# Optimization experiments

Measured on AMD Instinct MI355X. Metric: run time of the kernel, lower is better.

The kernel has to match this reference:

```python
import jax, jax.numpy as jnp
import numpy as np

N, E, D = 100000, 1280000, 64


def setup_inputs() -> dict:
    key = jax.random.key(0)
    ks = jax.random.split(key, 9)
    x = jax.random.normal(ks[0], (N, D), jnp.float32)
    edge_index = jax.random.randint(ks[1], (2, E), 0, N, dtype=jnp.int64)
    edge_weight = jax.random.uniform(ks[2], (E,), jnp.float32)
    s = 1.0 / np.sqrt(D)
    W0 = jax.random.normal(ks[3], (D, D), jnp.float32) * s
    b0 = jnp.zeros((D,), jnp.float32)
    W1 = jax.random.normal(ks[4], (D, D), jnp.float32) * s
    b1 = jnp.zeros((D,), jnp.float32)
    W2 = jax.random.normal(ks[5], (D, D), jnp.float32) * s
    b2 = jnp.zeros((D,), jnp.float32)
    return {"x": x, "edge_index": edge_index, "edge_weight": edge_weight,
            "W0": W0, "b0": b0, "W1": W1, "b1": b1, "W2": W2, "b2": b2}


def reference(x, edge_index, edge_weight, W0, b0, W1, b1, W2, b2):
    n = x.shape[0]
    row, col = edge_index[0], edge_index[1]
    # GCN normalization with self-loops (PyG gcn_norm, fill_value=1)
    loop = jnp.arange(n)
    row_f = jnp.concatenate([row, loop])
    col_f = jnp.concatenate([col, loop])
    w_f = jnp.concatenate([edge_weight, jnp.ones((n,), x.dtype)])
    deg = jax.ops.segment_sum(w_f, col_f, num_segments=n)
    dinv = jnp.where(deg > 0, jax.lax.rsqrt(deg), 0.0).astype(x.dtype)
    norm = dinv[row_f] * w_f * dinv[col_f]  # [E+N]

    def conv(h, W, b):
        h = h @ W                                  # [N, D_out]
        msg = h[row_f] * norm[:, None]             # gather + scale
        return jax.ops.segment_sum(msg, col_f, num_segments=n) + b

    results = [x]
    h = jax.nn.relu(conv(x, W0, b0))   # dropout p=0 / eval -> identity
    results.append(h)
    h = jax.nn.relu(conv(h, W1, b1))
    results.append(h)
    h = conv(h, W2, b2)                # last layer: no activation
    results.append(h)
    return tuple(results)
```

## Files before the change

### kernel.cpp

```cpp
#include <hip/hip_runtime.h>


#define TPB 256
#define P1_CHUNK 8192
#define DSH 7
#define DNB 128
#define STAGE_CAP 4096

__global__ __launch_bounds__(TPB) void k_p0(const int* __restrict__ col,
                                            int* __restrict__ chist, int E, int nbk) {
    __shared__ int h[1024];
    int tid = threadIdx.x;
    for (int i = tid; i < nbk; i += TPB) h[i] = 0;
    __syncthreads();
    int s0 = blockIdx.x * P1_CHUNK;
    int s1 = min(s0 + P1_CHUNK, E);
    for (int i = s0 + tid; i < s1; i += TPB) atomicAdd(&h[col[i] >> DSH], 1);
    __syncthreads();
    for (int i = tid; i < nbk; i += TPB)
        if (h[i]) atomicAdd(&chist[i], h[i]);
}

__global__ __launch_bounds__(1024) void k_scanb(const int* __restrict__ chist,
                                                int* __restrict__ cbase,
                                                int* __restrict__ ccur, int nbk, int E) {
    __shared__ int s[1024];
    int tid = threadIdx.x;
    int v = (tid < nbk) ? chist[tid] : 0;
    s[tid] = v;
    __syncthreads();
    for (int off = 1; off < 1024; off <<= 1) {
        int t = (tid >= off) ? s[tid - off] : 0;
        __syncthreads();
        s[tid] += t;
        __syncthreads();
    }
    if (tid < nbk) { int ex = s[tid] - v; cbase[tid] = ex; ccur[tid] = ex; }
    if (tid == 0) cbase[nbk] = E;
}

__global__ __launch_bounds__(TPB) void k_p1(const int* __restrict__ row,
                                            const int* __restrict__ col,
                                            const float* __restrict__ w,
                                            int* __restrict__ ccur,
                                            int2* __restrict__ bkt, int E, int nbk) {
    __shared__ int h[1024];
    __shared__ int base[1024];
    int tid = threadIdx.x;
    for (int i = tid; i < nbk; i += TPB) h[i] = 0;
    __syncthreads();
    int s0 = blockIdx.x * P1_CHUNK;
    int s1 = min(s0 + P1_CHUNK, E);
    for (int i = s0 + tid; i < s1; i += TPB) atomicAdd(&h[col[i] >> DSH], 1);
    __syncthreads();
    for (int i = tid; i < nbk; i += TPB) {
        int c = h[i];
        base[i] = c ? atomicAdd(&ccur[i], c) : 0;
        h[i] = 0;
    }
    __syncthreads();
    for (int i = s0 + tid; i < s1; i += TPB) {
        int c = col[i];
        int b = c >> DSH;
        int r = atomicAdd(&h[b], 1);
        bkt[base[b] + r] = make_int2(row[i] | ((c & (DNB - 1)) << 20), __float_as_int(w[i]));
    }
}

__global__ __launch_bounds__(TPB) void k_p2(const int2* __restrict__ bkt,
                                            const int* __restrict__ cbase,
                                            int* __restrict__ starts,
                                            int2* __restrict__ edges,
                                            float* __restrict__ dinv, int n, int E) {
    __shared__ int hist[DNB];
    __shared__ int curs[DNB];
    __shared__ int sc[DNB];
    __shared__ int2 stage[STAGE_CAP];
    int tid = threadIdx.x;
    int b = blockIdx.x;
    int s0 = cbase[b], s1 = cbase[b + 1];
    int cnt = s1 - s0;
    int nodeBase = b << DSH;
    if (tid < DNB) hist[tid] = 0;
    __syncthreads();
    for (int i = s0 + tid; i < s1; i += TPB)
        atomicAdd(&hist[(unsigned)bkt[i].x >> 20], 1);
    __syncthreads();
    int v = 0;
    if (tid < DNB) { v = hist[tid]; sc[tid] = v; }
    __syncthreads();
    for (int off = 1; off < DNB; off <<= 1) {
        int t = 0;
        if (tid < DNB && tid >= off) t = sc[tid - off];
        __syncthreads();
        if (tid < DNB) sc[tid] += t;
        __syncthreads();
    }
    if (tid < DNB) {
        int ex = sc[tid] - v;
        curs[tid] = ex;
        int node = nodeBase + tid;
        if (node < n) starts[node] = s0 + ex;
    }
    if (b == 0 && tid == 0) starts[n] = E;
    __syncthreads();
    if (cnt <= STAGE_CAP) {
        for (int i = s0 + tid; i < s1; i += TPB) {
            int2 ed = bkt[i];
            int d = (unsigned)ed.x >> 20;
            int r = atomicAdd(&curs[d], 1);
            stage[r] = make_int2(ed.x & 0xFFFFF, ed.y);
        }
        __syncthreads();
        for (int i = tid; i < cnt; i += TPB) edges[s0 + i] = stage[i];
        if (tid < DNB) {
            int node = nodeBase + tid;
            if (node < n) {
                float d = 1.0f;
                for (int j = sc[tid] - v; j < sc[tid]; ++j)
                    d += __int_as_float(stage[j].y);
                dinv[node] = rsqrtf(d);
            }
        }
    } else {
        for (int i = s0 + tid; i < s1; i += TPB) {
            int2 ed = bkt[i];
            int d = (unsigned)ed.x >> 20;
            int r = atomicAdd(&curs[d], 1);
            edges[s0 + r] = make_int2(ed.x & 0xFFFFF, ed.y);
        }
        __syncthreads();
        if (tid < DNB) {
            int node = nodeBase + tid;
            if (node < n) {
                float d = 1.0f;
                for (int j = sc[tid] - v; j < sc[tid]; ++j)
                    d += __int_as_float(edges[s0 + j].y);
                dinv[node] = rsqrtf(d);
            }
        }
    }
}

__global__ __launch_bounds__(TPB) void k_normcsr(const int* __restrict__ starts,
                                                 const float* __restrict__ dinv,
                                                 int2* __restrict__ edges, int n) {
    int i = blockIdx.x * TPB + threadIdx.x;
    if (i >= n) return;
    int s0 = starts[i], s1 = starts[i + 1];
    float dn = dinv[i];
    for (int s = s0; s < s1; ++s) {
        int2 ed = edges[s];
        edges[s].y = __float_as_int(dinv[ed.x] * __int_as_float(ed.y) * dn);
    }
}

__global__ __launch_bounds__(TPB, 3) void k_gemm64(const float* __restrict__ in,
                                                   const float* __restrict__ Wg,
                                                   float* __restrict__ out, int n) {
    __shared__ float4 Ws[1024];
    __shared__ float4 As[2048];
    int tid = threadIdx.x;
    const float4* Wf4 = (const float4*)Wg;
    #pragma unroll
    for (int i = 0; i < 4; ++i) Ws[i * 256 + tid] = Wf4[i * 256 + tid];
    int rowbase = blockIdx.x * 128;
    const float4* Af4 = (const float4*)in;
    #pragma unroll
    for (int i = 0; i < 8; ++i) {
        int f4 = i * 256 + tid;
        int r = f4 >> 4, c4 = f4 & 15;
        float4 v = make_float4(0.f, 0.f, 0.f, 0.f);
        if (rowbase + r < n) v = Af4[(size_t)(rowbase + r) * 16 + c4];
        As[r * 16 + (c4 ^ ((r >> 3) & 3))] = v;
    }
    __syncthreads();
    int jg = tid & 15;
    int rg = tid >> 4;
    int r0 = rg * 8;
    int sw = rg & 3;
    float4 acc[8];
    #pragma unroll
    for (int rr = 0; rr < 8; ++rr) acc[rr] = make_float4(0.f, 0.f, 0.f, 0.f);
    #pragma unroll 2
    for (int kt = 0; kt < 16; ++kt) {
        float4 w0 = Ws[(kt * 4 + 0) * 16 + jg];
        float4 w1 = Ws[(kt * 4 + 1) * 16 + jg];
        float4 w2 = Ws[(kt * 4 + 2) * 16 + jg];
        float4 w3 = Ws[(kt * 4 + 3) * 16 + jg];
        int ac = kt ^ sw;
        #pragma unroll
        for (int rr = 0; rr < 8; ++rr) {
            float4 a = As[(r0 + rr) * 16 + ac];
            acc[rr].x = fmaf(a.x, w0.x, acc[rr].x);
            acc[rr].y = fmaf(a.x, w0.y, acc[rr].y);
            acc[rr].z = fmaf(a.x, w0.z, acc[rr].z);
            acc[rr].w = fmaf(a.x, w0.w, acc[rr].w);
            acc[rr].x = fmaf(a.y, w1.x, acc[rr].x);
            acc[rr].y = fmaf(a.y, w1.y, acc[rr].y);
            acc[rr].z = fmaf(a.y, w1.z, acc[rr].z);
            acc[rr].w = fmaf(a.y, w1.w, acc[rr].w);
            acc[rr].x = fmaf(a.z, w2.x, acc[rr].x);
            acc[rr].y = fmaf(a.z, w2.y, acc[rr].y);
            acc[rr].z = fmaf(a.z, w2.z, acc[rr].z);
            acc[rr].w = fmaf(a.z, w2.w, acc[rr].w);
            acc[rr].x = fmaf(a.w, w3.x, acc[rr].x);
            acc[rr].y = fmaf(a.w, w3.y, acc[rr].y);
            acc[rr].z = fmaf(a.w, w3.z, acc[rr].z);
            acc[rr].w = fmaf(a.w, w3.w, acc[rr].w);
        }
    }
    #pragma unroll
    for (int rr = 0; rr < 8; ++rr) {
        int r = rowbase + r0 + rr;
        if (r < n) *(float4*)&out[(size_t)r * 64 + jg * 4] = acc[rr];
    }
}

__global__ __launch_bounds__(TPB) void k_gather(const int* __restrict__ starts,
                                                const int2* __restrict__ edges,
                                                const float* __restrict__ hw,
                                                const float* __restrict__ dinv,
                                                const float* __restrict__ b,
                                                float* __restrict__ out,
                                                int n, int relu) {
    int idx = blockIdx.x * TPB + threadIdx.x;
    int node = idx >> 4;
    if (node >= n) return;
    int f = (idx & 15) << 2;
    int s0 = starts[node], s1 = starts[node + 1];
    float di = dinv[node];
    float sc = di * di;
    float4 hself = *(const float4*)&hw[(size_t)node * 64 + f];
    float4 bb = *(const float4*)&b[f];
    float4 acc;
    acc.x = fmaf(hself.x, sc, bb.x);
    acc.y = fmaf(hself.y, sc, bb.y);
    acc.z = fmaf(hself.z, sc, bb.z);
    acc.w = fmaf(hself.w, sc, bb.w);
    int e = s0;
    for (; e + 4 <= s1; e += 4) {
        int2 e0 = edges[e + 0];
        int2 e1 = edges[e + 1];
        int2 e2 = edges[e + 2];
        int2 e3 = edges[e + 3];
        float4 h0 = *(const float4*)&hw[(size_t)e0.x * 64 + f];
        float4 h1 = *(const float4*)&hw[(size_t)e1.x * 64 + f];
        float4 h2 = *(const float4*)&hw[(size_t)e2.x * 64 + f];
        float4 h3 = *(const float4*)&hw[(size_t)e3.x * 64 + f];
        float n0 = __int_as_float(e0.y), n1 = __int_as_float(e1.y);
        float n2 = __int_as_float(e2.y), n3 = __int_as_float(e3.y);
        acc.x = fmaf(h0.x, n0, acc.x); acc.y = fmaf(h0.y, n0, acc.y);
        acc.z = fmaf(h0.z, n0, acc.z); acc.w = fmaf(h0.w, n0, acc.w);
        acc.x = fmaf(h1.x, n1, acc.x); acc.y = fmaf(h1.y, n1, acc.y);
        acc.z = fmaf(h1.z, n1, acc.z); acc.w = fmaf(h1.w, n1, acc.w);
        acc.x = fmaf(h2.x, n2, acc.x); acc.y = fmaf(h2.y, n2, acc.y);
        acc.z = fmaf(h2.z, n2, acc.z); acc.w = fmaf(h2.w, n2, acc.w);
        acc.x = fmaf(h3.x, n3, acc.x); acc.y = fmaf(h3.y, n3, acc.y);
        acc.z = fmaf(h3.z, n3, acc.z); acc.w = fmaf(h3.w, n3, acc.w);
    }
    for (; e < s1; ++e) {
        int2 ed = edges[e];
        float nm = __int_as_float(ed.y);
        float4 h = *(const float4*)&hw[(size_t)ed.x * 64 + f];
        acc.x = fmaf(h.x, nm, acc.x);
        acc.y = fmaf(h.y, nm, acc.y);
        acc.z = fmaf(h.z, nm, acc.z);
        acc.w = fmaf(h.w, nm, acc.w);
    }
    if (relu) {
        acc.x = acc.x > 0.f ? acc.x : 0.f;
        acc.y = acc.y > 0.f ? acc.y : 0.f;
        acc.z = acc.z > 0.f ? acc.z : 0.f;
        acc.w = acc.w > 0.f ? acc.w : 0.f;
    }
    *(float4*)&out[(size_t)node * 64 + f] = acc;
}

extern "C" void kernel_launch(void* const* d_in, const int* in_sizes, int n_in,
                              void* d_out, int out_size, void* d_ws, size_t ws_size,
                              hipStream_t stream) {
    const float* x = (const float*)d_in[0];
    const int* ei = (const int*)d_in[1];
    const float* ew = (const float*)d_in[2];
    const float* Wl[3] = {(const float*)d_in[3], (const float*)d_in[5], (const float*)d_in[7]};
    const float* Bl[3] = {(const float*)d_in[4], (const float*)d_in[6], (const float*)d_in[8]};

    const int n = in_sizes[0] / 64;
    const int E = in_sizes[2];
    const int* row = ei;
    const int* col = ei + E;
    float* out = (float*)d_out;

    const int nbk = (n + DNB - 1) >> DSH;
    const int p1b = (E + P1_CHUNK - 1) / P1_CHUNK;

    char* ws = (char*)d_ws;
    size_t o = 0;
    float* dinv  = (float*)(ws + o);  o = (o + (size_t)n * 4 + 255) & ~(size_t)255;
    float* hw    = (float*)(ws + o);
    int2*  bkt   = (int2*)(ws + o);   o = (o + (size_t)n * 256 + 255) & ~(size_t)255;
    int* starts  = (int*)(ws + o);    o = (o + (size_t)(n + 1) * 4 + 255) & ~(size_t)255;
    int* chist   = (int*)(ws + o);    o = (o + 1024 * 4 + 255) & ~(size_t)255;
    int* cbase   = (int*)(ws + o);    o = (o + 1025 * 4 + 255) & ~(size_t)255;
    int* ccur    = (int*)(ws + o);    o = (o + 1024 * 4 + 255) & ~(size_t)255;
    int2* edges  = (int2*)(ws + o);

    hipMemcpyAsync(out, x, (size_t)n * 64 * sizeof(float), hipMemcpyDeviceToDevice, stream);

    hipMemsetAsync(chist, 0, (size_t)nbk * 4, stream);
    k_p0<<<p1b, TPB, 0, stream>>>(col, chist, E, nbk);
    k_scanb<<<1, 1024, 0, stream>>>(chist, cbase, ccur, nbk, E);
    k_p1<<<p1b, TPB, 0, stream>>>(row, col, ew, ccur, bkt, E, nbk);
    k_p2<<<nbk, TPB, 0, stream>>>(bkt, cbase, starts, edges, dinv, n, E);
    k_normcsr<<<(n + TPB - 1) / TPB, TPB, 0, stream>>>(starts, dinv, edges, n);

    const float* hin = x;
    for (int L = 0; L < 3; ++L) {
        float* oseg = out + (size_t)(L + 1) * n * 64;
        k_gemm64<<<(n + 127) / 128, TPB, 0, stream>>>(hin, Wl[L], hw, n);
        k_gather<<<(n * 16 + TPB - 1) / TPB, TPB, 0, stream>>>(starts, edges, hw, dinv, Bl[L], oseg, n, L < 2 ? 1 : 0);
        hin = oseg;
    }
}
```

Measured before the change: 438.7 us.

## Split gather edges across 4 slots per node, drop normcsr pass and x copy

The gather kernel now gives each node a full 64-lane wavefront, with 4 edge slots of 16 lanes each. The partial sums are combined with cross-lane shuffles. The per-edge normalisation kernel is removed: the source dinv is applied inside the gather and the destination dinv is applied once per node after the reduction, which adds an extra dinv gather per edge. The device-to-device copy of x into the output is folded into the first GEMM's load phase, so the separate memcpy launch and the extra pass over memory go away.

Result: no change. 434.0 us (-1.1%).

```diff
diff --git a/kernel.cpp b/kernel.cpp
--- a/kernel.cpp
+++ b/kernel.cpp
@@ -142,22 +142,10 @@
     }
 }
 
-__global__ __launch_bounds__(TPB) void k_normcsr(const int* __restrict__ starts,
-                                                 const float* __restrict__ dinv,
-                                                 int2* __restrict__ edges, int n) {
-    int i = blockIdx.x * TPB + threadIdx.x;
-    if (i >= n) return;
-    int s0 = starts[i], s1 = starts[i + 1];
-    float dn = dinv[i];
-    for (int s = s0; s < s1; ++s) {
-        int2 ed = edges[s];
-        edges[s].y = __float_as_int(dinv[ed.x] * __int_as_float(ed.y) * dn);
-    }
-}
-
 __global__ __launch_bounds__(TPB, 3) void k_gemm64(const float* __restrict__ in,
                                                    const float* __restrict__ Wg,
-                                                   float* __restrict__ out, int n) {
+                                                   float* __restrict__ out,
+                                                   float* __restrict__ cp, int n) {
     __shared__ float4 Ws[1024];
     __shared__ float4 As[2048];
     int tid = threadIdx.x;
@@ -171,7 +159,10 @@
         int f4 = i * 256 + tid;
         int r = f4 >> 4, c4 = f4 & 15;
         float4 v = make_float4(0.f, 0.f, 0.f, 0.f);
-        if (rowbase + r < n) v = Af4[(size_t)(rowbase + r) * 16 + c4];
+        if (rowbase + r < n) {
+            v = Af4[(size_t)(rowbase + r) * 16 + c4];
+            if (cp) *(float4*)&cp[((size_t)(rowbase + r) * 16 + c4) * 4] = v;
+        }
         As[r * 16 + (c4 ^ ((r >> 3) & 3))] = v;
     }
     __syncthreads();
@@ -224,57 +215,68 @@
                                                 const float* __restrict__ b,
                                                 float* __restrict__ out,
                                                 int n, int relu) {
-    int idx = blockIdx.x * TPB + threadIdx.x;
-    int node = idx >> 4;
+    int node = blockIdx.x * 4 + (threadIdx.x >> 6);
     if (node >= n) return;
-    int f = (idx & 15) << 2;
+    int lane = threadIdx.x & 63;
+    int eslot = lane >> 4;
+    int f = (lane & 15) << 2;
     int s0 = starts[node], s1 = starts[node + 1];
-    float di = dinv[node];
-    float sc = di * di;
-    float4 hself = *(const float4*)&hw[(size_t)node * 64 + f];
-    float4 bb = *(const float4*)&b[f];
-    float4 acc;
-    acc.x = fmaf(hself.x, sc, bb.x);
-    acc.y = fmaf(hself.y, sc, bb.y);
-    acc.z = fmaf(hself.z, sc, bb.z);
-    acc.w = fmaf(hself.w, sc, bb.w);
-    int e = s0;
-    for (; e + 4 <= s1; e += 4) {
-        int2 e0 = edges[e + 0];
-        int2 e1 = edges[e + 1];
-        int2 e2 = edges[e + 2];
-        int2 e3 = edges[e + 3];
-        float4 h0 = *(const float4*)&hw[(size_t)e0.x * 64 + f];
-        float4 h1 = *(const float4*)&hw[(size_t)e1.x * 64 + f];
-        float4 h2 = *(const float4*)&hw[(size_t)e2.x * 64 + f];
-        float4 h3 = *(const float4*)&hw[(size_t)e3.x * 64 + f];
-        float n0 = __int_as_float(e0.y), n1 = __int_as_float(e1.y);
-        float n2 = __int_as_float(e2.y), n3 = __int_as_float(e3.y);
-        acc.x = fmaf(h0.x, n0, acc.x); acc.y = fmaf(h0.y, n0, acc.y);
-        acc.z = fmaf(h0.z, n0, acc.z); acc.w = fmaf(h0.w, n0, acc.w);
-        acc.x = fmaf(h1.x, n1, acc.x); acc.y = fmaf(h1.y, n1, acc.y);
-        acc.z = fmaf(h1.z, n1, acc.z); acc.w = fmaf(h1.w, n1, acc.w);
-        acc.x = fmaf(h2.x, n2, acc.x); acc.y = fmaf(h2.y, n2, acc.y);
-        acc.z = fmaf(h2.z, n2, acc.z); acc.w = fmaf(h2.w, n2, acc.w);
-        acc.x = fmaf(h3.x, n3, acc.x); acc.y = fmaf(h3.y, n3, acc.y);
-        acc.z = fmaf(h3.z, n3, acc.z); acc.w = fmaf(h3.w, n3, acc.w);
-    }
-    for (; e < s1; ++e) {
+    float4 acc = make_float4(0.f, 0.f, 0.f, 0.f);
+    int e = s0 + eslot;
+    for (; e + 4 < s1; e += 8) {
+        int2 ed0 = edges[e];
+        int2 ed1 = edges[e + 4];
+        float nm0 = dinv[ed0.x] * __int_as_float(ed0.y);
+        float nm1 = dinv[ed1.x] * __int_as_float(ed1.y);
+        float4 h0 = *(const float4*)&hw[(size_t)ed0.x * 64 + f];
+        float4 h1 = *(const float4*)&hw[(size_t)ed1.x * 64 + f];
+        acc.x = fmaf(h0.x, nm0, acc.x);
+        acc.y = fmaf(h0.y, nm0, acc.y);
+        acc.z = fmaf(h0.z, nm0, acc.z);
+        acc.w = fmaf(h0.w, nm0, acc.w);
+        acc.x = fmaf(h1.x, nm1, acc.x);
+        acc.y = fmaf(h1.y, nm1, acc.y);
+        acc.z = fmaf(h1.z, nm1, acc.z);
+        acc.w = fmaf(h1.w, nm1, acc.w);
+    }
+    if (e < s1) {
         int2 ed = edges[e];
-        float nm = __int_as_float(ed.y);
+        float nm = dinv[ed.x] * __int_as_float(ed.y);
         float4 h = *(const float4*)&hw[(size_t)ed.x * 64 + f];
         acc.x = fmaf(h.x, nm, acc.x);
         acc.y = fmaf(h.y, nm, acc.y);
         acc.z = fmaf(h.z, nm, acc.z);
         acc.w = fmaf(h.w, nm, acc.w);
     }
-    if (relu) {
-        acc.x = acc.x > 0.f ? acc.x : 0.f;
-        acc.y = acc.y > 0.f ? acc.y : 0.f;
-        acc.z = acc.z > 0.f ? acc.z : 0.f;
-        acc.w = acc.w > 0.f ? acc.w : 0.f;
-    }
-    *(float4*)&out[(size_t)node * 64 + f] = acc;
+    acc.x += __shfl_xor(acc.x, 16);
+    acc.y += __shfl_xor(acc.y, 16);
+    acc.z += __shfl_xor(acc.z, 16);
+    acc.w += __shfl_xor(acc.w, 16);
+    acc.x += __shfl_xor(acc.x, 32);
+    acc.y += __shfl_xor(acc.y, 32);
+    acc.z += __shfl_xor(acc.z, 32);
+    acc.w += __shfl_xor(acc.w, 32);
+    if (eslot == 0) {
+        float di = dinv[node];
+        float4 hs = *(const float4*)&hw[(size_t)node * 64 + f];
+        float4 bb = *(const float4*)&b[f];
+        float ix = fmaf(hs.x, di, acc.x);
+        float iy = fmaf(hs.y, di, acc.y);
+        float iz = fmaf(hs.z, di, acc.z);
+        float iw = fmaf(hs.w, di, acc.w);
+        float4 o;
+        o.x = fmaf(ix, di, bb.x);
+        o.y = fmaf(iy, di, bb.y);
+        o.z = fmaf(iz, di, bb.z);
+        o.w = fmaf(iw, di, bb.w);
+        if (relu) {
+            o.x = o.x > 0.f ? o.x : 0.f;
+            o.y = o.y > 0.f ? o.y : 0.f;
+            o.z = o.z > 0.f ? o.z : 0.f;
+            o.w = o.w > 0.f ? o.w : 0.f;
+        }
+        *(float4*)&out[(size_t)node * 64 + f] = o;
+    }
 }
 
 extern "C" void kernel_launch(void* const* d_in, const int* in_sizes, int n_in,
@@ -306,20 +308,17 @@
     int* ccur    = (int*)(ws + o);    o = (o + 1024 * 4 + 255) & ~(size_t)255;
     int2* edges  = (int2*)(ws + o);
 
-    hipMemcpyAsync(out, x, (size_t)n * 64 * sizeof(float), hipMemcpyDeviceToDevice, stream);
-
     hipMemsetAsync(chist, 0, (size_t)nbk * 4, stream);
     k_p0<<<p1b, TPB, 0, stream>>>(col, chist, E, nbk);
     k_scanb<<<1, 1024, 0, stream>>>(chist, cbase, ccur, nbk, E);
     k_p1<<<p1b, TPB, 0, stream>>>(row, col, ew, ccur, bkt, E, nbk);
     k_p2<<<nbk, TPB, 0, stream>>>(bkt, cbase, starts, edges, dinv, n, E);
-    k_normcsr<<<(n + TPB - 1) / TPB, TPB, 0, stream>>>(starts, dinv, edges, n);
 
     const float* hin = x;
     for (int L = 0; L < 3; ++L) {
         float* oseg = out + (size_t)(L + 1) * n * 64;
-        k_gemm64<<<(n + 127) / 128, TPB, 0, stream>>>(hin, Wl[L], hw, n);
-        k_gather<<<(n * 16 + TPB - 1) / TPB, TPB, 0, stream>>>(starts, edges, hw, dinv, Bl[L], oseg, n, L < 2 ? 1 : 0);
+        k_gemm64<<<(n + 127) / 128, TPB, 0, stream>>>(hin, Wl[L], hw, L == 0 ? out : nullptr, n);
+        k_gather<<<(n + 3) / 4, TPB, 0, stream>>>(starts, edges, hw, dinv, Bl[L], oseg, n, L < 2 ? 1 : 0);
         hin = oseg;
     }
 }
```
